# Kernel tuning notes

Measured on AMD Instinct MI355X. Metric: run time of the kernel, lower is better.

Reference implementation:

```python
import jax, jax.numpy as jnp
import numpy as np

N = 64
H_IN = W_IN = 512
K = 9
H_OUT = H_IN - (K - 1)  # 504 (stride=1, dilation=1, no padding)
W_OUT = W_IN - (K - 1)  # 504


def setup_inputs() -> dict:
    key = jax.random.key(0)
    k1, k2, k3 = jax.random.split(key, 3)
    x = jax.random.normal(k1, (N, H_IN, W_IN), dtype=jnp.float32)
    # torch.rand -> uniform [0,1)
    weight = jax.random.uniform(k2, (H_OUT, W_OUT, K, K), dtype=jnp.float32)
    bias = jax.random.uniform(k3, (H_OUT, W_OUT), dtype=jnp.float32)
    return {"x": x, "weight": weight, "bias": bias}


def reference(x, weight, bias):
    # Locally connected 2D (no weight sharing):
    #   y[n,h,w] = sum_{i,j} x[n, h+i, w+j] * weight[h, w, i, j] + bias[h, w]
    # Equivalent to the original unfold + einsum('nklhw,hwkl->nhw'), but we
    # accumulate over the small fixed k*k taps with static slices instead of
    # materializing the huge [N,k,k,H_out,W_out] patch tensor.
    acc = jnp.zeros((x.shape[0], H_OUT, W_OUT), dtype=x.dtype)
    for i in range(K):
        for j in range(K):
            acc = acc + x[:, i:i + H_OUT, j:j + W_OUT] * weight[None, :, :, i, j]
    y = acc + bias[None, :, :]
    return jax.nn.relu(y)
```

## Files before the change

### kernel.cpp

```cpp
#include <hip/hip_runtime.h>


#define H_IN 512
#define W_IN 512
#define H_OUT 504
#define W_OUT 504
#define W_T 8
#define H_T 4
#define TROWS (H_T + 8)
#define XF (TROWS * 1024)

__device__ __forceinline__ float readlane_f(float v, int l) {
    return __int_as_float(__builtin_amdgcn_readlane(__float_as_int(v), l));
}

__launch_bounds__(256, 3)
__global__ void lc2d_kernel(const float* __restrict__ x,
                            const float* __restrict__ weight,
                            const float* __restrict__ bias,
                            float* __restrict__ out) {
    __shared__ float lds[XF];

    const int t    = threadIdx.x;
    const int lane = t & 63;
    const int wv   = t >> 6;

    const int h0 = blockIdx.y * H_T;
    const int w0 = blockIdx.x * W_T;

    {
        const int n  = t >> 2;
        const int wq = t & 3;
        const float* gx = x + (size_t)n * (H_IN * W_IN)
                            + (size_t)h0 * W_IN + w0 + wq * 4;
        float* ld = &lds[wq * 256 + ((n * 4) ^ (wq * 4))];
        #pragma unroll
        for (int row = 0; row < TROWS; ++row) {
            const float4 v = *reinterpret_cast<const float4*>(gx + row * W_IN);
            *reinterpret_cast<float4*>(ld + row * 1024) = v;
        }
    }

    float wpk[18];
    {
        const float* wb = weight + ((size_t)(h0 + wv) * W_OUT + w0) * 81;
        const int qb = lane >> 4;
        const int rr = lane & 15;
        #pragma unroll
        for (int d = 0; d < 18; ++d) {
            const int q  = 4 * d + qb;
            const int k  = q / 9;
            const int tp = q - 9 * k;
            float v = 0.f;
            if (rr < 9) v = wb[k * 81 + rr * 9 + tp];
            wpk[d] = v;
        }
    }

    __syncthreads();

    const int wvu = __builtin_amdgcn_readfirstlane(wv);
    const int h   = h0 + wvu;

    float acc[W_T];
    {
        const float* bptr = bias + (size_t)h * W_OUT + w0;
        #pragma unroll
        for (int k = 0; k < W_T; ++k) acc[k] = bptr[k];
    }

    const float* xp0 = &lds[0 * 256 + ((lane * 4) ^ 0)  + wvu * 1024];
    const float* xp1 = &lds[1 * 256 + ((lane * 4) ^ 4)  + wvu * 1024];
    const float* xp2 = &lds[2 * 256 + ((lane * 4) ^ 8)  + wvu * 1024];
    const float* xp3 = &lds[3 * 256 + ((lane * 4) ^ 12) + wvu * 1024];

    #pragma unroll 1
    for (int r = 0; r < 9; ++r) {
        float xr[16];
        {
            const float4 v0 = *reinterpret_cast<const float4*>(xp0);
            const float4 v1 = *reinterpret_cast<const float4*>(xp1);
            const float4 v2 = *reinterpret_cast<const float4*>(xp2);
            const float4 v3 = *reinterpret_cast<const float4*>(xp3);
            xr[0] = v0.x; xr[1] = v0.y; xr[2]  = v0.z; xr[3]  = v0.w;
            xr[4] = v1.x; xr[5] = v1.y; xr[6]  = v1.z; xr[7]  = v1.w;
            xr[8] = v2.x; xr[9] = v2.y; xr[10] = v2.z; xr[11] = v2.w;
            xr[12] = v3.x; xr[13] = v3.y; xr[14] = v3.z; xr[15] = v3.w;
        }

        const int li0 = r;
        const int li1 = r + 16;
        const int li2 = r + 32;
        const int li3 = r + 48;

        #pragma unroll
        for (int tp = 0; tp < 9; ++tp) {
            #pragma unroll
            for (int k = 0; k < W_T; ++k) {
                const int q  = k * 9 + tp;
                const int qm = q & 3;
                const int li = (qm == 0) ? li0 : (qm == 1) ? li1
                             : (qm == 2) ? li2 : li3;
                const float w = readlane_f(wpk[q >> 2], li);
                acc[k] = fmaf(w, xr[k + tp], acc[k]);
            }
        }

        xp0 += 1024; xp1 += 1024; xp2 += 1024; xp3 += 1024;
    }

    float* o = out + (size_t)lane * (H_OUT * W_OUT) + (size_t)h * W_OUT + w0;
    float4 s;
    s.x = fmaxf(acc[0], 0.f); s.y = fmaxf(acc[1], 0.f);
    s.z = fmaxf(acc[2], 0.f); s.w = fmaxf(acc[3], 0.f);
    *reinterpret_cast<float4*>(o) = s;
    s.x = fmaxf(acc[4], 0.f); s.y = fmaxf(acc[5], 0.f);
    s.z = fmaxf(acc[6], 0.f); s.w = fmaxf(acc[7], 0.f);
    *reinterpret_cast<float4*>(o + 4) = s;
}

extern "C" void kernel_launch(void* const* d_in, const int* in_sizes, int n_in,
                              void* d_out, int out_size, void* d_ws, size_t ws_size,
                              hipStream_t stream) {
    const float* x      = (const float*)d_in[0];
    const float* weight = (const float*)d_in[1];
    const float* bias   = (const float*)d_in[2];
    float* out          = (float*)d_out;

    dim3 grid(W_OUT / W_T, H_OUT / H_T);
    dim3 block(256);
    lc2d_kernel<<<grid, block, 0, stream>>>(x, weight, bias, out);
}
```

Measured before the change: 290.9 us.

## Make kernel persistent with register-prefetched next tile and nontemporal loads/stores

Replaces the one-tile-per-block grid with 768 persistent blocks that each walk a contiguous range of tiles. While computing the current tile, each block prefetches the next tile's x rows and weights into registers, then copies them into LDS between two barriers. It also uses nontemporal loads for the weights and nontemporal stores for the output. The aim is to hide global-load latency behind compute and cut launch and tail overhead, at the cost of much higher register pressure (48 extra floats for rx plus wnx) under launch_bounds(256,3), and an extra barrier per tile.

```diff
diff --git a/kernel.cpp b/kernel.cpp
--- a/kernel.cpp
+++ b/kernel.cpp
@@ -9,6 +9,12 @@
 #define H_T 4
 #define TROWS (H_T + 8)
 #define XF (TROWS * 1024)
+#define NTX 63
+#define NTY 126
+#define NT (NTX * NTY)
+#define NBLK 768
+
+typedef float f4v __attribute__((ext_vector_type(4)));
 
 __device__ __forceinline__ float readlane_f(float v, int l) {
     return __int_as_float(__builtin_amdgcn_readlane(__float_as_int(v), l));
@@ -24,99 +30,131 @@
     const int t    = threadIdx.x;
     const int lane = t & 63;
     const int wv   = t >> 6;
+    const int wvu  = __builtin_amdgcn_readfirstlane(wv);
 
-    const int h0 = blockIdx.y * H_T;
-    const int w0 = blockIdx.x * W_T;
+    int tile       = (int)(((long long)blockIdx.x * NT) / NBLK);
+    const int tend = (int)(((long long)(blockIdx.x + 1) * NT) / NBLK);
 
-    {
-        const int n  = t >> 2;
-        const int wq = t & 3;
-        const float* gx = x + (size_t)n * (H_IN * W_IN)
-                            + (size_t)h0 * W_IN + w0 + wq * 4;
-        float* ld = &lds[wq * 256 + ((n * 4) ^ (wq * 4))];
+    const int sn   = t >> 2;
+    const int swq  = t & 3;
+    const int sswz = swq * 256 + ((sn * 4) ^ (swq * 4));
+
+    const int qb = lane >> 4;
+    const int rr = lane & 15;
+
+    float4 rx[12];
+    float  wpk[18];
+    float  wnx[18];
+
+    auto issue = [&](int tl) {
+        const int tx = tl / NTY;
+        const int ty = tl - tx * NTY;
+        const int h0 = ty * H_T;
+        const int w0 = tx * W_T;
+        const float* gx = x + (size_t)sn * (H_IN * W_IN)
+                            + (size_t)h0 * W_IN + w0 + swq * 4;
         #pragma unroll
-        for (int row = 0; row < TROWS; ++row) {
-            const float4 v = *reinterpret_cast<const float4*>(gx + row * W_IN);
-            *reinterpret_cast<float4*>(ld + row * 1024) = v;
+        for (int row = 0; row < TROWS; ++row)
+            rx[row] = *reinterpret_cast<const float4*>(gx + row * W_IN);
+        if (rr < 9) {
+            const float* wb = weight + ((size_t)(h0 + wv) * W_OUT + w0) * 81;
+            #pragma unroll
+            for (int d = 0; d < 18; ++d) {
+                const int q  = 4 * d + qb;
+                const int k  = q / 9;
+                const int tp = q - 9 * k;
+                wnx[d] = __builtin_nontemporal_load(wb + k * 81 + rr * 9 + tp);
+            }
         }
-    }
+    };
 
-    float wpk[18];
-    {
-        const float* wb = weight + ((size_t)(h0 + wv) * W_OUT + w0) * 81;
-        const int qb = lane >> 4;
-        const int rr = lane & 15;
-        #pragma unroll
-        for (int d = 0; d < 18; ++d) {
-            const int q  = 4 * d + qb;
-            const int k  = q / 9;
-            const int tp = q - 9 * k;
-            float v = 0.f;
-            if (rr < 9) v = wb[k * 81 + rr * 9 + tp];
-            wpk[d] = v;
-        }
-    }
-
+    issue(tile);
+    #pragma unroll
+    for (int row = 0; row < TROWS; ++row)
+        *reinterpret_cast<float4*>(&lds[row * 1024 + sswz]) = rx[row];
+    #pragma unroll
+    for (int d = 0; d < 18; ++d) wpk[d] = wnx[d];
     __syncthreads();
 
-    const int wvu = __builtin_amdgcn_readfirstlane(wv);
-    const int h   = h0 + wvu;
+    while (tile < tend) {
+        const int nx = (tile + 1 < tend) ? tile + 1 : tile;
+        issue(nx);
 
-    float acc[W_T];
-    {
-        const float* bptr = bias + (size_t)h * W_OUT + w0;
-        #pragma unroll
-        for (int k = 0; k < W_T; ++k) acc[k] = bptr[k];
-    }
+        const int tx = tile / NTY;
+        const int ty = tile - tx * NTY;
+        const int h0 = ty * H_T;
+        const int w0 = tx * W_T;
+        const int h  = h0 + wvu;
 
-    const float* xp0 = &lds[0 * 256 + ((lane * 4) ^ 0)  + wvu * 1024];
-    const float* xp1 = &lds[1 * 256 + ((lane * 4) ^ 4)  + wvu * 1024];
-    const float* xp2 = &lds[2 * 256 + ((lane * 4) ^ 8)  + wvu * 1024];
-    const float* xp3 = &lds[3 * 256 + ((lane * 4) ^ 12) + wvu * 1024];
-
-    #pragma unroll 1
-    for (int r = 0; r < 9; ++r) {
-        float xr[16];
+        float acc[W_T];
         {
-            const float4 v0 = *reinterpret_cast<const float4*>(xp0);
-            const float4 v1 = *reinterpret_cast<const float4*>(xp1);
-            const float4 v2 = *reinterpret_cast<const float4*>(xp2);
-            const float4 v3 = *reinterpret_cast<const float4*>(xp3);
-            xr[0] = v0.x; xr[1] = v0.y; xr[2]  = v0.z; xr[3]  = v0.w;
-            xr[4] = v1.x; xr[5] = v1.y; xr[6]  = v1.z; xr[7]  = v1.w;
-            xr[8] = v2.x; xr[9] = v2.y; xr[10] = v2.z; xr[11] = v2.w;
-            xr[12] = v3.x; xr[13] = v3.y; xr[14] = v3.z; xr[15] = v3.w;
+            const float* bptr = bias + (size_t)h * W_OUT + w0;
+            #pragma unroll
+            for (int k = 0; k < W_T; ++k) acc[k] = bptr[k];
         }
 
-        const int li0 = r;
-        const int li1 = r + 16;
-        const int li2 = r + 32;
-        const int li3 = r + 48;
+        const float* xp0 = &lds[0 * 256 + ((lane * 4) ^ 0)  + wvu * 1024];
+        const float* xp1 = &lds[1 * 256 + ((lane * 4) ^ 4)  + wvu * 1024];
+        const float* xp2 = &lds[2 * 256 + ((lane * 4) ^ 8)  + wvu * 1024];
+        const float* xp3 = &lds[3 * 256 + ((lane * 4) ^ 12) + wvu * 1024];
 
-        #pragma unroll
-        for (int tp = 0; tp < 9; ++tp) {
+        #pragma unroll 1
+        for (int r = 0; r < 9; ++r) {
+            float xr[16];
+            {
+                const float4 v0 = *reinterpret_cast<const float4*>(xp0);
+                const float4 v1 = *reinterpret_cast<const float4*>(xp1);
+                const float4 v2 = *reinterpret_cast<const float4*>(xp2);
+                const float4 v3 = *reinterpret_cast<const float4*>(xp3);
+                xr[0]  = v0.x; xr[1]  = v0.y; xr[2]  = v0.z; xr[3]  = v0.w;
+                xr[4]  = v1.x; xr[5]  = v1.y; xr[6]  = v1.z; xr[7]  = v1.w;
+                xr[8]  = v2.x; xr[9]  = v2.y; xr[10] = v2.z; xr[11] = v2.w;
+                xr[12] = v3.x; xr[13] = v3.y; xr[14] = v3.z; xr[15] = v3.w;
+            }
+
+            const int li0 = r;
+            const int li1 = r + 16;
+            const int li2 = r + 32;
+            const int li3 = r + 48;
+
             #pragma unroll
-            for (int k = 0; k < W_T; ++k) {
-                const int q  = k * 9 + tp;
-                const int qm = q & 3;
-                const int li = (qm == 0) ? li0 : (qm == 1) ? li1
-                             : (qm == 2) ? li2 : li3;
-                const float w = readlane_f(wpk[q >> 2], li);
-                acc[k] = fmaf(w, xr[k + tp], acc[k]);
+            for (int tp = 0; tp < 9; ++tp) {
+                #pragma unroll
+                for (int k = 0; k < W_T; ++k) {
+                    const int q  = k * 9 + tp;
+                    const int qm = q & 3;
+                    const int li = (qm == 0) ? li0 : (qm == 1) ? li1
+                                 : (qm == 2) ? li2 : li3;
+                    const float w = readlane_f(wpk[q >> 2], li);
+                    acc[k] = fmaf(w, xr[k + tp], acc[k]);
+                }
             }
+
+            xp0 += 1024; xp1 += 1024; xp2 += 1024; xp3 += 1024;
         }
 
-        xp0 += 1024; xp1 += 1024; xp2 += 1024; xp3 += 1024;
+        {
+            float* o = out + (size_t)lane * (H_OUT * W_OUT)
+                           + (size_t)h * W_OUT + w0;
+            f4v s;
+            s.x = fmaxf(acc[0], 0.f); s.y = fmaxf(acc[1], 0.f);
+            s.z = fmaxf(acc[2], 0.f); s.w = fmaxf(acc[3], 0.f);
+            __builtin_nontemporal_store(s, reinterpret_cast<f4v*>(o));
+            s.x = fmaxf(acc[4], 0.f); s.y = fmaxf(acc[5], 0.f);
+            s.z = fmaxf(acc[6], 0.f); s.w = fmaxf(acc[7], 0.f);
+            __builtin_nontemporal_store(s, reinterpret_cast<f4v*>(o + 4));
+        }
+
+        __syncthreads();
+        #pragma unroll
+        for (int row = 0; row < TROWS; ++row)
+            *reinterpret_cast<float4*>(&lds[row * 1024 + sswz]) = rx[row];
+        #pragma unroll
+        for (int d = 0; d < 18; ++d) wpk[d] = wnx[d];
+        __syncthreads();
+
+        ++tile;
     }
-
-    float* o = out + (size_t)lane * (H_OUT * W_OUT) + (size_t)h * W_OUT + w0;
-    float4 s;
-    s.x = fmaxf(acc[0], 0.f); s.y = fmaxf(acc[1], 0.f);
-    s.z = fmaxf(acc[2], 0.f); s.w = fmaxf(acc[3], 0.f);
-    *reinterpret_cast<float4*>(o) = s;
-    s.x = fmaxf(acc[4], 0.f); s.y = fmaxf(acc[5], 0.f);
-    s.z = fmaxf(acc[6], 0.f); s.w = fmaxf(acc[7], 0.f);
-    *reinterpret_cast<float4*>(o + 4) = s;
 }
 
 extern "C" void kernel_launch(void* const* d_in, const int* in_sizes, int n_in,
@@ -127,7 +165,7 @@
     const float* bias   = (const float*)d_in[2];
     float* out          = (float*)d_out;
 
-    dim3 grid(W_OUT / W_T, H_OUT / H_T);
+    dim3 grid(NBLK);
     dim3 block(256);
     lc2d_kernel<<<grid, block, 0, stream>>>(x, weight, bias, out);
 }
```

New measurement: 480.6 us. 1.65x slower.

## Double row tile to 8, use 512-thread blocks with XCD-aware block swizzle

Applied to the files above, without the earlier changes.

Doubles the output rows per block from 4 to 8 and uses 512 threads (8 waves), so the 8-row halo of the x tile is shared across more output rows and each block re-reads less input from global memory. Blocks are launched on a 1D grid and remapped so that consecutive tiles land on the same XCD, with column-major tile order to improve L2 locality. Weight loads switch to nontemporal hints because weights are used only once. The LDS tile grows to 16 rows (64 KB), which may limit how many blocks fit per CU.

```diff
diff --git a/kernel.cpp b/kernel.cpp
--- a/kernel.cpp
+++ b/kernel.cpp
@@ -6,15 +6,18 @@
 #define H_OUT 504
 #define W_OUT 504
 #define W_T 8
-#define H_T 4
+#define H_T 8
 #define TROWS (H_T + 8)
 #define XF (TROWS * 1024)
+#define NTX 63
+#define NTY 63
+#define NBLK (NTX * NTY)
 
 __device__ __forceinline__ float readlane_f(float v, int l) {
     return __int_as_float(__builtin_amdgcn_readlane(__float_as_int(v), l));
 }
 
-__launch_bounds__(256, 3)
+__launch_bounds__(512, 4)
 __global__ void lc2d_kernel(const float* __restrict__ x,
                             const float* __restrict__ weight,
                             const float* __restrict__ bias,
@@ -25,19 +28,31 @@
     const int lane = t & 63;
     const int wv   = t >> 6;
 
-    const int h0 = blockIdx.y * H_T;
-    const int w0 = blockIdx.x * W_T;
+    int swz;
+    {
+        const int bid = blockIdx.x;
+        const int xcd = bid & 7, i = bid >> 3;
+        const int q = NBLK >> 3, r = NBLK & 7;
+        swz = (xcd < r ? xcd * (q + 1)
+                       : r * (q + 1) + (xcd - r) * q) + i;
+    }
+    const int ty = swz % NTY;
+    const int tx = swz / NTY;
+    const int h0 = ty * H_T;
+    const int w0 = tx * W_T;
 
     {
-        const int n  = t >> 2;
-        const int wq = t & 3;
+        const int n  = t >> 3;
+        const int c  = t & 7;
+        const int wq = c & 3;
+        const int rp = c >> 2;
         const float* gx = x + (size_t)n * (H_IN * W_IN)
-                            + (size_t)h0 * W_IN + w0 + wq * 4;
-        float* ld = &lds[wq * 256 + ((n * 4) ^ (wq * 4))];
+                            + (size_t)(h0 + rp) * W_IN + w0 + wq * 4;
+        float* ld = &lds[rp * 1024 + wq * 256 + ((n * 4) ^ (wq * 4))];
         #pragma unroll
-        for (int row = 0; row < TROWS; ++row) {
-            const float4 v = *reinterpret_cast<const float4*>(gx + row * W_IN);
-            *reinterpret_cast<float4*>(ld + row * 1024) = v;
+        for (int rep = 0; rep < 8; ++rep) {
+            const float4 v = *reinterpret_cast<const float4*>(gx + rep * 2 * W_IN);
+            *reinterpret_cast<float4*>(ld + rep * 2048) = v;
         }
     }
 
@@ -52,7 +67,7 @@
             const int k  = q / 9;
             const int tp = q - 9 * k;
             float v = 0.f;
-            if (rr < 9) v = wb[k * 81 + rr * 9 + tp];
+            if (rr < 9) v = __builtin_nontemporal_load(wb + k * 81 + rr * 9 + tp);
             wpk[d] = v;
         }
     }
@@ -82,9 +97,9 @@
             const float4 v1 = *reinterpret_cast<const float4*>(xp1);
             const float4 v2 = *reinterpret_cast<const float4*>(xp2);
             const float4 v3 = *reinterpret_cast<const float4*>(xp3);
-            xr[0] = v0.x; xr[1] = v0.y; xr[2]  = v0.z; xr[3]  = v0.w;
-            xr[4] = v1.x; xr[5] = v1.y; xr[6]  = v1.z; xr[7]  = v1.w;
-            xr[8] = v2.x; xr[9] = v2.y; xr[10] = v2.z; xr[11] = v2.w;
+            xr[0]  = v0.x; xr[1]  = v0.y; xr[2]  = v0.z; xr[3]  = v0.w;
+            xr[4]  = v1.x; xr[5]  = v1.y; xr[6]  = v1.z; xr[7]  = v1.w;
+            xr[8]  = v2.x; xr[9]  = v2.y; xr[10] = v2.z; xr[11] = v2.w;
             xr[12] = v3.x; xr[13] = v3.y; xr[14] = v3.z; xr[15] = v3.w;
         }
 
@@ -127,7 +142,7 @@
     const float* bias   = (const float*)d_in[2];
     float* out          = (float*)d_out;
 
-    dim3 grid(W_OUT / W_T, H_OUT / H_T);
-    dim3 block(256);
+    dim3 grid(NBLK);
+    dim3 block(512);
     lc2d_kernel<<<grid, block, 0, stream>>>(x, weight, bias, out);
 }
```

Result: slower. 305.4 us (+5.0%).

## Persist blocks over row tiles with ring-buffered LDS and prefetched weights

Applied to the files above, without the earlier changes.

Turns the kernel persistent: each block walks a vertical segment of row tiles using a 16-row circular LDS buffer. Each step loads only the 4 new input rows, so the 8-row halo is no longer reloaded per tile. The next tile's rows and weights are prefetched into registers while the current tile computes, and weight loads become nontemporal. It launches far fewer blocks (504) with lower occupancy (launch bounds 2), adds a barrier per tile, and raises register pressure.

```diff
diff --git a/kernel.cpp b/kernel.cpp
--- a/kernel.cpp
+++ b/kernel.cpp
@@ -7,14 +7,18 @@
 #define W_OUT 504
 #define W_T 8
 #define H_T 4
-#define TROWS (H_T + 8)
-#define XF (TROWS * 1024)
+#define NTX 63
+#define NTYT 126
+#define NSEG 8
+#define NBLK (NSEG * NTX)
+#define RS 16
+#define XF (RS * 1024)
 
 __device__ __forceinline__ float readlane_f(float v, int l) {
     return __int_as_float(__builtin_amdgcn_readlane(__float_as_int(v), l));
 }
 
-__launch_bounds__(256, 3)
+__launch_bounds__(256, 2)
 __global__ void lc2d_kernel(const float* __restrict__ x,
                             const float* __restrict__ weight,
                             const float* __restrict__ bias,
@@ -24,99 +28,147 @@
     const int t    = threadIdx.x;
     const int lane = t & 63;
     const int wv   = t >> 6;
+    const int wvu  = __builtin_amdgcn_readfirstlane(wv);
 
-    const int h0 = blockIdx.y * H_T;
-    const int w0 = blockIdx.x * W_T;
+    const int col = blockIdx.x % NTX;
+    const int seg = blockIdx.x / NTX;
+    const int ty0 = (seg * NTYT) / NSEG;
+    const int ty1 = ((seg + 1) * NTYT) / NSEG;
+    const int w0  = col * W_T;
+
+    const int sn   = t >> 2;
+    const int swq  = t & 3;
+    const int sof  = swq * 256 + ((sn * 4) ^ (swq * 4));
+    const float* gxb = x + (size_t)sn * (H_IN * W_IN) + w0 + swq * 4;
+
+    const int qb = lane >> 4;
+    const int rr = lane & 15;
 
     {
-        const int n  = t >> 2;
-        const int wq = t & 3;
-        const float* gx = x + (size_t)n * (H_IN * W_IN)
-                            + (size_t)h0 * W_IN + w0 + wq * 4;
-        float* ld = &lds[wq * 256 + ((n * 4) ^ (wq * 4))];
+        const int hb = ty0 * H_T;
         #pragma unroll
-        for (int row = 0; row < TROWS; ++row) {
-            const float4 v = *reinterpret_cast<const float4*>(gx + row * W_IN);
-            *reinterpret_cast<float4*>(ld + row * 1024) = v;
+        for (int rrow = 0; rrow < 12; ++rrow) {
+            const int hrow = hb + rrow;
+            const float4 v = *reinterpret_cast<const float4*>(
+                gxb + (size_t)hrow * W_IN);
+            *reinterpret_cast<float4*>(&lds[(hrow & 15) * 1024 + sof]) = v;
         }
     }
-
     float wpk[18];
     {
-        const float* wb = weight + ((size_t)(h0 + wv) * W_OUT + w0) * 81;
-        const int qb = lane >> 4;
-        const int rr = lane & 15;
+        const float* wb = weight + ((size_t)(ty0 * H_T + wv) * W_OUT + w0) * 81;
         #pragma unroll
         for (int d = 0; d < 18; ++d) {
             const int q  = 4 * d + qb;
             const int k  = q / 9;
             const int tp = q - 9 * k;
             float v = 0.f;
-            if (rr < 9) v = wb[k * 81 + rr * 9 + tp];
+            if (rr < 9) v = __builtin_nontemporal_load(wb + k * 81 + rr * 9 + tp);
             wpk[d] = v;
         }
     }
-
     __syncthreads();
 
-    const int wvu = __builtin_amdgcn_readfirstlane(wv);
-    const int h   = h0 + wvu;
+    const int lo0 = 0 * 256 + ((lane * 4) ^ 0);
+    const int lo1 = 1 * 256 + ((lane * 4) ^ 4);
+    const int lo2 = 2 * 256 + ((lane * 4) ^ 8);
+    const int lo3 = 3 * 256 + ((lane * 4) ^ 12);
 
-    float acc[W_T];
-    {
-        const float* bptr = bias + (size_t)h * W_OUT + w0;
-        #pragma unroll
-        for (int k = 0; k < W_T; ++k) acc[k] = bptr[k];
-    }
+    for (int ty = ty0; ty < ty1; ++ty) {
+        const int h0   = ty * H_T;
+        const bool more = (ty + 1 < ty1);
 
-    const float* xp0 = &lds[0 * 256 + ((lane * 4) ^ 0)  + wvu * 1024];
-    const float* xp1 = &lds[1 * 256 + ((lane * 4) ^ 4)  + wvu * 1024];
-    const float* xp2 = &lds[2 * 256 + ((lane * 4) ^ 8)  + wvu * 1024];
-    const float* xp3 = &lds[3 * 256 + ((lane * 4) ^ 12) + wvu * 1024];
-
-    #pragma unroll 1
-    for (int r = 0; r < 9; ++r) {
-        float xr[16];
-        {
-            const float4 v0 = *reinterpret_cast<const float4*>(xp0);
-            const float4 v1 = *reinterpret_cast<const float4*>(xp1);
-            const float4 v2 = *reinterpret_cast<const float4*>(xp2);
-            const float4 v3 = *reinterpret_cast<const float4*>(xp3);
-            xr[0] = v0.x; xr[1] = v0.y; xr[2]  = v0.z; xr[3]  = v0.w;
-            xr[4] = v1.x; xr[5] = v1.y; xr[6]  = v1.z; xr[7]  = v1.w;
-            xr[8] = v2.x; xr[9] = v2.y; xr[10] = v2.z; xr[11] = v2.w;
-            xr[12] = v3.x; xr[13] = v3.y; xr[14] = v3.z; xr[15] = v3.w;
+        float4 rxa, rxb, rxc, rxd;
+        if (more) {
+            rxa = *reinterpret_cast<const float4*>(gxb + (size_t)(h0 + 12) * W_IN);
+            rxb = *reinterpret_cast<const float4*>(gxb + (size_t)(h0 + 13) * W_IN);
+            rxc = *reinterpret_cast<const float4*>(gxb + (size_t)(h0 + 14) * W_IN);
+            rxd = *reinterpret_cast<const float4*>(gxb + (size_t)(h0 + 15) * W_IN);
         }
-
-        const int li0 = r;
-        const int li1 = r + 16;
-        const int li2 = r + 32;
-        const int li3 = r + 48;
-
-        #pragma unroll
-        for (int tp = 0; tp < 9; ++tp) {
+        float wnx[18];
+        if (more) {
+            const float* wb = weight + ((size_t)(h0 + 4 + wv) * W_OUT + w0) * 81;
             #pragma unroll
-            for (int k = 0; k < W_T; ++k) {
-                const int q  = k * 9 + tp;
-                const int qm = q & 3;
-                const int li = (qm == 0) ? li0 : (qm == 1) ? li1
-                             : (qm == 2) ? li2 : li3;
-                const float w = readlane_f(wpk[q >> 2], li);
-                acc[k] = fmaf(w, xr[k + tp], acc[k]);
+            for (int d = 0; d < 18; ++d) {
+                const int q  = 4 * d + qb;
+                const int k  = q / 9;
+                const int tp = q - 9 * k;
+                float v = 0.f;
+                if (rr < 9)
+                    v = __builtin_nontemporal_load(wb + k * 81 + rr * 9 + tp);
+                wnx[d] = v;
             }
         }
 
-        xp0 += 1024; xp1 += 1024; xp2 += 1024; xp3 += 1024;
+        const int h  = h0 + wvu;
+        const int hb = h;
+
+        float acc[W_T];
+        {
+            const float* bptr = bias + (size_t)h * W_OUT + w0;
+            #pragma unroll
+            for (int k = 0; k < W_T; ++k) acc[k] = bptr[k];
+        }
+
+        #pragma unroll 1
+        for (int r = 0; r < 9; ++r) {
+            const int sl = ((hb + r) & 15) * 1024;
+
+            float xr[16];
+            {
+                const float4 v0 = *reinterpret_cast<const float4*>(&lds[sl + lo0]);
+                const float4 v1 = *reinterpret_cast<const float4*>(&lds[sl + lo1]);
+                const float4 v2 = *reinterpret_cast<const float4*>(&lds[sl + lo2]);
+                const float4 v3 = *reinterpret_cast<const float4*>(&lds[sl + lo3]);
+                xr[0]  = v0.x; xr[1]  = v0.y; xr[2]  = v0.z; xr[3]  = v0.w;
+                xr[4]  = v1.x; xr[5]  = v1.y; xr[6]  = v1.z; xr[7]  = v1.w;
+                xr[8]  = v2.x; xr[9]  = v2.y; xr[10] = v2.z; xr[11] = v2.w;
+                xr[12] = v3.x; xr[13] = v3.y; xr[14] = v3.z; xr[15] = v3.w;
+            }
+
+            const int li0 = r;
+            const int li1 = r + 16;
+            const int li2 = r + 32;
+            const int li3 = r + 48;
+
+            #pragma unroll
+            for (int tp = 0; tp < 9; ++tp) {
+                #pragma unroll
+                for (int k = 0; k < W_T; ++k) {
+                    const int q  = k * 9 + tp;
+                    const int qm = q & 3;
+                    const int li = (qm == 0) ? li0 : (qm == 1) ? li1
+                                 : (qm == 2) ? li2 : li3;
+                    const float w = readlane_f(wpk[q >> 2], li);
+                    acc[k] = fmaf(w, xr[k + tp], acc[k]);
+                }
+            }
+        }
+
+        {
+            float* o = out + (size_t)lane * (H_OUT * W_OUT)
+                           + (size_t)h * W_OUT + w0;
+            float4 s;
+            s.x = fmaxf(acc[0], 0.f); s.y = fmaxf(acc[1], 0.f);
+            s.z = fmaxf(acc[2], 0.f); s.w = fmaxf(acc[3], 0.f);
+            *reinterpret_cast<float4*>(o) = s;
+            s.x = fmaxf(acc[4], 0.f); s.y = fmaxf(acc[5], 0.f);
+            s.z = fmaxf(acc[6], 0.f); s.w = fmaxf(acc[7], 0.f);
+            *reinterpret_cast<float4*>(o + 4) = s;
+        }
+
+        if (more) {
+            *reinterpret_cast<float4*>(&lds[((h0 + 12) & 15) * 1024 + sof]) = rxa;
+            *reinterpret_cast<float4*>(&lds[((h0 + 13) & 15) * 1024 + sof]) = rxb;
+            *reinterpret_cast<float4*>(&lds[((h0 + 14) & 15) * 1024 + sof]) = rxc;
+            *reinterpret_cast<float4*>(&lds[((h0 + 15) & 15) * 1024 + sof]) = rxd;
+        }
+        __syncthreads();
+        if (more) {
+            #pragma unroll
+            for (int d = 0; d < 18; ++d) wpk[d] = wnx[d];
+        }
     }
-
-    float* o = out + (size_t)lane * (H_OUT * W_OUT) + (size_t)h * W_OUT + w0;
-    float4 s;
-    s.x = fmaxf(acc[0], 0.f); s.y = fmaxf(acc[1], 0.f);
-    s.z = fmaxf(acc[2], 0.f); s.w = fmaxf(acc[3], 0.f);
-    *reinterpret_cast<float4*>(o) = s;
-    s.x = fmaxf(acc[4], 0.f); s.y = fmaxf(acc[5], 0.f);
-    s.z = fmaxf(acc[6], 0.f); s.w = fmaxf(acc[7], 0.f);
-    *reinterpret_cast<float4*>(o + 4) = s;
 }
 
 extern "C" void kernel_launch(void* const* d_in, const int* in_sizes, int n_in,
@@ -127,7 +179,7 @@
     const float* bias   = (const float*)d_in[2];
     float* out          = (float*)d_out;
 
-    dim3 grid(W_OUT / W_T, H_OUT / H_T);
+    dim3 grid(NBLK);
     dim3 block(256);
     lc2d_kernel<<<grid, block, 0, stream>>>(x, weight, bias, out);
 }
```

Result: slower. 308.9 us (+6.2%).
